# Kernel optimization log

Measured on AMD Instinct MI355X. Metric: run time of the kernel, lower is better.

Reference implementation:

```python
import jax, jax.numpy as jnp
import numpy as np
import math

FOV, NEAR, FAR = 60.0, 0.1, 100.0
W_RES, H_RES = 128, 128
N_GAUSS = 1024


def _normalize(v):
    return v / (jnp.linalg.norm(v) + 1e-8)


def _view_matrix(pos, look_at, up):
    # Same construction as Camera._compute_view_matrix
    f = _normalize(look_at - pos)
    r = _normalize(jnp.cross(f, up))
    u = _normalize(jnp.cross(r, f))
    return jnp.stack([
        jnp.concatenate([r, -jnp.dot(r, pos)[None]]),
        jnp.concatenate([u, -jnp.dot(u, pos)[None]]),
        jnp.concatenate([-f, jnp.dot(f, pos)[None]]),
        jnp.array([0.0, 0.0, 0.0, 1.0], dtype=pos.dtype),
    ])


def _proj_matrix():
    # Same construction as Camera._compute_projection_matrix
    aspect = W_RES / H_RES
    foc = 1.0 / math.tan(math.radians(FOV) / 2.0)
    P = np.zeros((4, 4), np.float32)
    P[0, 0] = foc / aspect
    P[1, 1] = foc
    P[2, 2] = (FAR + NEAR) / (NEAR - FAR)
    P[2, 3] = 2.0 * FAR * NEAR / (NEAR - FAR)
    P[3, 2] = -1.0
    return jnp.asarray(P)


def _quat_to_rot(q):
    # q: [N,4] (w,x,y,z) -> [N,3,3]
    q = q / (jnp.linalg.norm(q, axis=-1, keepdims=True) + 1e-8)
    w, x, y, z = q[:, 0], q[:, 1], q[:, 2], q[:, 3]
    return jnp.stack([
        jnp.stack([1 - 2 * (y * y + z * z), 2 * (x * y - w * z), 2 * (x * z + w * y)], -1),
        jnp.stack([2 * (x * y + w * z), 1 - 2 * (x * x + z * z), 2 * (y * z - w * x)], -1),
        jnp.stack([2 * (x * z - w * y), 2 * (y * z + w * x), 1 - 2 * (x * x + y * y)], -1),
    ], axis=1)


def _splat(means, log_scales, quats, opacity_logits, colors, cam_position, look_at, up):
    V = _view_matrix(cam_position, look_at, up)
    P = _proj_matrix()

    # 3D covariance: R S S^T R^T
    R = _quat_to_rot(quats)                       # [N,3,3]
    S = jnp.exp(log_scales)                       # [N,3]
    M = R * S[:, None, :]
    cov3d = jnp.einsum('nij,nkj->nik', M, M)      # [N,3,3]

    # Project means to view / clip / pixel space
    mh = jnp.concatenate([means, jnp.ones((means.shape[0], 1), means.dtype)], -1)
    pv = mh @ V.T                                 # [N,4] view space
    tx, ty, tz = pv[:, 0], pv[:, 1], pv[:, 2]     # tz < 0 in front of camera
    depth = -tz
    clip = pv @ P.T
    cw = jnp.where(jnp.abs(clip[:, 3]) < 1e-6, 1e-6, clip[:, 3])
    ndc = clip[:, :2] / cw[:, None]
    px = (ndc[:, 0] + 1.0) * 0.5 * W_RES          # pixel x center
    py = (ndc[:, 1] + 1.0) * 0.5 * H_RES          # pixel y center

    # EWA Jacobian -> 2D covariance
    foc = 1.0 / math.tan(math.radians(FOV) / 2.0)
    fx = foc / (W_RES / H_RES) * (W_RES / 2.0)
    fy = foc * (H_RES / 2.0)
    zsafe = jnp.where(jnp.abs(tz) < 1e-6, 1e-6, tz)
    zero = jnp.zeros_like(zsafe)
    J = jnp.stack([
        jnp.stack([fx / zsafe, zero, -fx * tx / (zsafe * zsafe)], -1),
        jnp.stack([zero, fy / zsafe, -fy * ty / (zsafe * zsafe)], -1),
    ], axis=1)                                    # [N,2,3]
    T = jnp.einsum('nij,jk->nik', J, V[:3, :3])   # [N,2,3]
    cov2d = jnp.einsum('nij,njk,nlk->nil', T, cov3d, T)  # [N,2,2]
    a = cov2d[:, 0, 0] + 0.3
    b = cov2d[:, 0, 1]
    c = cov2d[:, 1, 1] + 0.3
    det = jnp.maximum(a * c - b * b, 1e-6)
    ia, ib, ic = c / det, -b / det, a / det       # inverse 2x2

    # Per-pixel Gaussian weights: [N,H,W]
    u = jnp.arange(W_RES, dtype=means.dtype) + 0.5
    v = jnp.arange(H_RES, dtype=means.dtype) + 0.5
    dx = px[:, None, None] - u[None, None, :]
    dy = py[:, None, None] - v[None, :, None]
    power = -0.5 * (ia[:, None, None] * dx * dx
                    + 2.0 * ib[:, None, None] * dx * dy
                    + ic[:, None, None] * dy * dy)
    opac = jax.nn.sigmoid(opacity_logits)
    w = opac[:, None, None] * jnp.exp(jnp.minimum(power, 0.0))
    valid = (depth > NEAR) & (depth < FAR)
    w = jnp.where(valid[:, None, None], w, 0.0)
    w = jnp.clip(w, 0.0, 0.99)

    # Depth sort (front-to-back) then alpha composite via exclusive cumsum of log(1-a)
    order = jnp.argsort(depth)
    ws = w[order]                                 # [N,H,W]
    cs = jax.nn.sigmoid(colors)[order]            # [N,3]
    ds = depth[order]
    log_om = jnp.log1p(-ws)
    trans = jnp.exp(jnp.cumsum(log_om, axis=0) - log_om)  # exclusive transmittance
    contrib = trans * ws                          # [N,H,W]
    rgb = jnp.einsum('nhw,nc->chw', contrib, cs)  # [3,H,W]
    depth_img = jnp.sum(contrib * ds[:, None, None], axis=0, keepdims=True)
    alpha_img = jnp.sum(contrib, axis=0, keepdims=True)
    # background_color = [0,0,0] so no background term is added
    return rgb, depth_img, alpha_img


def setup_inputs() -> dict:
    key = jax.random.key(0)
    ks = jax.random.split(key, 6)
    means = jax.random.normal(ks[0], (N_GAUSS, 3), jnp.float32) * 1.5
    log_scales = jax.random.normal(ks[1], (N_GAUSS, 3), jnp.float32) * 0.3 - 2.5
    quats = jax.random.normal(ks[2], (N_GAUSS, 4), jnp.float32)
    opacity_logits = jax.random.normal(ks[3], (N_GAUSS,), jnp.float32)
    colors = jax.random.normal(ks[4], (N_GAUSS, 3), jnp.float32)
    cam_position = jnp.array([0.0, 0.0, 5.0], jnp.float32) + 0.05 * jax.random.normal(ks[5], (3,), jnp.float32)
    look_at = jnp.zeros((3,), jnp.float32)
    up = jnp.array([0.0, 1.0, 0.0], jnp.float32)
    return {"means": means, "log_scales": log_scales, "quats": quats,
            "opacity_logits": opacity_logits, "colors": colors,
            "cam_position": cam_position, "look_at": look_at, "up": up}


def reference(means, log_scales, quats, opacity_logits, colors, cam_position, look_at, up):
    return _splat(means, log_scales, quats, opacity_logits, colors, cam_position, look_at, up)
```

## Files before the change

### kernel.cpp

```cpp
#include <hip/hip_runtime.h>
#include <math.h>

#define NG 1024
#define W_RES 128
#define H_RES 128
#define NPIX (W_RES * H_RES)
#define NCHUNK 8
#define CH (NG / NCHUNK)
#define TILES_X 8
#define TILES_Y 8
#define NTILE (TILES_X * TILES_Y)

__device__ float  s_px[NG];
__device__ float  s_py[NG];
__device__ float  s_R2[NG];
__device__ float4 s_g0[NG];
__device__ float4 s_g1[NG];
__device__ float4 s_col[NG];
__device__ float  g_part[6 * NCHUNK * NPIX];

__global__ __launch_bounds__(128) void prep_kernel(
    const float* __restrict__ means, const float* __restrict__ log_scales,
    const float* __restrict__ quats, const float* __restrict__ opacity_logits,
    const float* __restrict__ colors, const float* __restrict__ cam,
    const float* __restrict__ look, const float* __restrict__ up) {
  __shared__ __align__(16) float sdepth[NG];
  const int tid = threadIdx.x;
  const int me = blockIdx.x * CH + tid;

  const float cpx = cam[0], cpy = cam[1], cpz = cam[2];
  float fx0 = look[0] - cpx, fy0 = look[1] - cpy, fz0 = look[2] - cpz;
  float inv = 1.f / (sqrtf(fx0 * fx0 + fy0 * fy0 + fz0 * fz0) + 1e-8f);
  const float fX = fx0 * inv, fY = fy0 * inv, fZ = fz0 * inv;
  const float ux0 = up[0], uy0 = up[1], uz0 = up[2];
  float rX0 = fY * uz0 - fZ * uy0, rY0 = fZ * ux0 - fX * uz0, rZ0 = fX * uy0 - fY * ux0;
  inv = 1.f / (sqrtf(rX0 * rX0 + rY0 * rY0 + rZ0 * rZ0) + 1e-8f);
  const float rX = rX0 * inv, rY = rY0 * inv, rZ = rZ0 * inv;
  float uX0 = rY * fZ - rZ * fY, uY0 = rZ * fX - rX * fZ, uZ0 = rX * fY - rY * fX;
  inv = 1.f / (sqrtf(uX0 * uX0 + uY0 * uY0 + uZ0 * uZ0) + 1e-8f);
  const float uX = uX0 * inv, uY = uY0 * inv, uZ = uZ0 * inv;
  const float V00 = rX, V01 = rY, V02 = rZ, V03 = -(rX * cpx + rY * cpy + rZ * cpz);
  const float V10 = uX, V11 = uY, V12 = uZ, V13 = -(uX * cpx + uY * cpy + uZ * cpz);
  const float V20 = -fX, V21 = -fY, V22 = -fZ, V23 = (fX * cpx + fY * cpy + fZ * cpz);

  const float foc = 1.7320508075688772f;
  const float fpx = foc * 64.f;
  const float fpy = foc * 64.f;

#pragma unroll
  for (int i = 0; i < NG / CH; ++i) {
    const int g = i * CH + tid;
    const float mx = means[3 * g + 0], my = means[3 * g + 1], mz = means[3 * g + 2];
    sdepth[g] = -(V20 * mx + V21 * my + V22 * mz + V23);
  }
  __syncthreads();

  const float dme = sdepth[me];
  int rank = 0;
  const float4* dep4 = (const float4*)sdepth;
#pragma unroll 4
  for (int k = 0; k < NG / 4; ++k) {
    const float4 d4 = dep4[k];
    const int j = 4 * k;
    rank += (d4.x < dme || (d4.x == dme && (j + 0) < me)) ? 1 : 0;
    rank += (d4.y < dme || (d4.y == dme && (j + 1) < me)) ? 1 : 0;
    rank += (d4.z < dme || (d4.z == dme && (j + 2) < me)) ? 1 : 0;
    rank += (d4.w < dme || (d4.w == dme && (j + 3) < me)) ? 1 : 0;
  }

  float qw = quats[4 * me + 0], qx = quats[4 * me + 1], qy = quats[4 * me + 2], qz = quats[4 * me + 3];
  float qinv = 1.f / (sqrtf(qw * qw + qx * qx + qy * qy + qz * qz) + 1e-8f);
  qw *= qinv; qx *= qinv; qy *= qinv; qz *= qinv;
  const float R00 = 1.f - 2.f * (qy * qy + qz * qz), R01 = 2.f * (qx * qy - qw * qz), R02 = 2.f * (qx * qz + qw * qy);
  const float R10 = 2.f * (qx * qy + qw * qz), R11 = 1.f - 2.f * (qx * qx + qz * qz), R12 = 2.f * (qy * qz - qw * qx);
  const float R20 = 2.f * (qx * qz - qw * qy), R21 = 2.f * (qy * qz + qw * qx), R22 = 1.f - 2.f * (qx * qx + qy * qy);
  const float s0 = __expf(log_scales[3 * me + 0]);
  const float s1 = __expf(log_scales[3 * me + 1]);
  const float s2 = __expf(log_scales[3 * me + 2]);
  const float M00 = R00 * s0, M01 = R01 * s1, M02 = R02 * s2;
  const float M10 = R10 * s0, M11 = R11 * s1, M12 = R12 * s2;
  const float M20 = R20 * s0, M21 = R21 * s1, M22 = R22 * s2;
  const float c00 = M00 * M00 + M01 * M01 + M02 * M02;
  const float c01 = M00 * M10 + M01 * M11 + M02 * M12;
  const float c02 = M00 * M20 + M01 * M21 + M02 * M22;
  const float c11 = M10 * M10 + M11 * M11 + M12 * M12;
  const float c12 = M10 * M20 + M11 * M21 + M12 * M22;
  const float c22 = M20 * M20 + M21 * M21 + M22 * M22;
  const float mx = means[3 * me + 0], my = means[3 * me + 1], mz = means[3 * me + 2];
  const float tx = V00 * mx + V01 * my + V02 * mz + V03;
  const float ty = V10 * mx + V11 * my + V12 * mz + V13;
  const float tz = V20 * mx + V21 * my + V22 * mz + V23;
  const float depth = -tz;
  const float cw = (fabsf(depth) < 1e-6f) ? 1e-6f : depth;
  const float pxs = (foc * tx / cw + 1.f) * 0.5f * (float)W_RES;
  const float pys = (foc * ty / cw + 1.f) * 0.5f * (float)H_RES;
  const float zs = (fabsf(tz) < 1e-6f) ? 1e-6f : tz;
  const float J00 = fpx / zs, J02 = -fpx * tx / (zs * zs);
  const float J11 = fpy / zs, J12 = -fpy * ty / (zs * zs);
  const float T00 = J00 * V00 + J02 * V20;
  const float T01 = J00 * V01 + J02 * V21;
  const float T02 = J00 * V02 + J02 * V22;
  const float T10 = J11 * V10 + J12 * V20;
  const float T11 = J11 * V11 + J12 * V21;
  const float T12 = J11 * V12 + J12 * V22;
  const float t00 = T00 * c00 + T01 * c01 + T02 * c02;
  const float t01 = T00 * c01 + T01 * c11 + T02 * c12;
  const float t02 = T00 * c02 + T01 * c12 + T02 * c22;
  const float t10 = T10 * c00 + T11 * c01 + T12 * c02;
  const float t11 = T10 * c01 + T11 * c11 + T12 * c12;
  const float t12 = T10 * c02 + T11 * c12 + T12 * c22;
  const float a  = t00 * T00 + t01 * T01 + t02 * T02 + 0.3f;
  const float bb = t00 * T10 + t01 * T11 + t02 * T12;
  const float c  = t10 * T10 + t11 * T11 + t12 * T12 + 0.3f;
  const float det = fmaxf(a * c - bb * bb, 1e-6f);
  const float ia = c / det, ib = -bb / det, ic = a / det;
  const float op = 1.f / (1.f + __expf(-opacity_logits[me]));
  const bool valid = (depth > 0.1f) && (depth < 100.f);
  const float lam = 0.5f * (a + c) + sqrtf(0.25f * (a - c) * (a - c) + bb * bb);
  float R2v = 2.f * lam * logf(op * 1e7f);
  if (!valid) R2v = -1.f;
  const float logop = logf(op);
  const float cr = 1.f / (1.f + __expf(-colors[3 * me + 0]));
  const float cg = 1.f / (1.f + __expf(-colors[3 * me + 1]));
  const float cb = 1.f / (1.f + __expf(-colors[3 * me + 2]));

  s_px[rank] = pxs;
  s_py[rank] = pys;
  s_R2[rank] = R2v;
  s_g0[rank] = make_float4(pxs, pys, -0.5f * ia, -ib);
  s_g1[rank] = make_float4(-0.5f * ic, logop, depth, 0.f);
  s_col[rank] = make_float4(cr, cg, cb, 0.f);
}

__global__ __launch_bounds__(256) void render_kernel() {
  __shared__ int slist[CH];
  __shared__ int scnt[2];
  __shared__ int stotal;
  const int tid = threadIdx.x;
  const int tile = blockIdx.x;
  const int chunk = blockIdx.y;
  const int ox = (tile & (TILES_X - 1)) * 16;
  const int oy = (tile >> 3) * 16;
  const float x0 = ox + 0.5f, x1 = ox + 15.5f;
  const float y0 = oy + 0.5f, y1 = oy + 15.5f;

  bool surv = false;
  if (tid < CH) {
    const int g = chunk * CH + tid;
    const float gx = s_px[g], gy = s_py[g], r2 = s_R2[g];
    const float nx = fminf(fmaxf(gx, x0), x1);
    const float ny = fminf(fmaxf(gy, y0), y1);
    const float ddx = nx - gx, ddy = ny - gy;
    surv = (ddx * ddx + ddy * ddy) <= r2;
  }
  const unsigned long long m = __ballot(surv);
  const int wid = tid >> 6, lane = tid & 63;
  if (tid < CH && lane == 0) scnt[wid] = __popcll(m);
  __syncthreads();
  if (surv) {
    const int base = (wid == 1) ? scnt[0] : 0;
    const int pos = base + __popcll(m & ((1ull << lane) - 1ull));
    slist[pos] = chunk * CH + tid;
  }
  if (tid == 0) stotal = scnt[0] + scnt[1];
  __syncthreads();
  const int ns = stotal;

  const int lx = tid & 15, ly = tid >> 4;
  const float u = (float)(ox + lx) + 0.5f;
  const float v = (float)(oy + ly) + 0.5f;
  float T = 1.f, ar = 0.f, ag = 0.f, ab = 0.f, ad = 0.f, aa = 0.f;
  for (int s = 0; s < ns; ++s) {
    const int g = slist[s];
    const float4 g0 = s_g0[g];
    const float4 g1 = s_g1[g];
    const float4 cc = s_col[g];
    const float dx = g0.x - u, dy = g0.y - v;
    float pw = dx * (g0.z * dx + g0.w * dy) + g1.x * dy * dy;
    pw = fminf(pw, 0.f) + g1.y;
    const float w = fminf(__expf(pw), 0.99f);
    const float ctr = T * w;
    ar += ctr * cc.x; ag += ctr * cc.y; ab += ctr * cc.z;
    ad += ctr * g1.z; aa += ctr;
    T *= (1.f - w);
  }
  const int p = (oy + ly) * W_RES + (ox + lx);
  const int idx = chunk * NPIX + p;
  g_part[0 * NCHUNK * NPIX + idx] = ar;
  g_part[1 * NCHUNK * NPIX + idx] = ag;
  g_part[2 * NCHUNK * NPIX + idx] = ab;
  g_part[3 * NCHUNK * NPIX + idx] = ad;
  g_part[4 * NCHUNK * NPIX + idx] = aa;
  g_part[5 * NCHUNK * NPIX + idx] = T;
}

__global__ __launch_bounds__(256) void combine_kernel(float* __restrict__ out) {
  const int p = blockIdx.x * 256 + threadIdx.x;
  float T = 1.f, r = 0.f, g = 0.f, b = 0.f, d = 0.f, a = 0.f;
#pragma unroll
  for (int ch = 0; ch < NCHUNK; ++ch) {
    const int idx = ch * NPIX + p;
    const float pr = g_part[0 * NCHUNK * NPIX + idx];
    const float pg = g_part[1 * NCHUNK * NPIX + idx];
    const float pb = g_part[2 * NCHUNK * NPIX + idx];
    const float pd = g_part[3 * NCHUNK * NPIX + idx];
    const float pa = g_part[4 * NCHUNK * NPIX + idx];
    const float pT = g_part[5 * NCHUNK * NPIX + idx];
    r += T * pr; g += T * pg; b += T * pb; d += T * pd; a += T * pa;
    T *= pT;
  }
  out[0 * NPIX + p] = r;
  out[1 * NPIX + p] = g;
  out[2 * NPIX + p] = b;
  out[3 * NPIX + p] = d;
  out[4 * NPIX + p] = a;
}

extern "C" void kernel_launch(void* const* d_in, const int* in_sizes, int n_in,
                              void* d_out, int out_size, void* d_ws, size_t ws_size,
                              hipStream_t stream) {
  const float* means = (const float*)d_in[0];
  const float* log_scales = (const float*)d_in[1];
  const float* quats = (const float*)d_in[2];
  const float* opacity_logits = (const float*)d_in[3];
  const float* colors = (const float*)d_in[4];
  const float* cam = (const float*)d_in[5];
  const float* look = (const float*)d_in[6];
  const float* up = (const float*)d_in[7];
  float* out = (float*)d_out;

  prep_kernel<<<NCHUNK, CH, 0, stream>>>(means, log_scales, quats, opacity_logits,
                                         colors, cam, look, up);
  render_kernel<<<dim3(NTILE, NCHUNK), 256, 0, stream>>>();
  combine_kernel<<<NPIX / 256, 256, 0, stream>>>(out);
}
```

Measured before the change: 106.9 us.

## Render each tile over all gaussians in one block, drop combine kernel

The render kernel no longer splits the gaussians into 8 chunks across blocks. Each tile block now culls all 1024 depth-sorted gaussians and compacts the survivors' parameters into shared memory. It then composites them and writes the final output directly, which removes the partial-result buffer and the combine kernel launch. The cost is only 64 blocks on a large GPU and a longer serial compositing loop per pixel, in exchange for one fewer launch, less global traffic and no indirect gather.

```diff
diff --git a/kernel.cpp b/kernel.cpp
--- a/kernel.cpp
+++ b/kernel.cpp
@@ -5,19 +5,15 @@
 #define W_RES 128
 #define H_RES 128
 #define NPIX (W_RES * H_RES)
-#define NCHUNK 8
-#define CH (NG / NCHUNK)
+#define NBLK 8
+#define BT (NG / NBLK)
 #define TILES_X 8
-#define TILES_Y 8
-#define NTILE (TILES_X * TILES_Y)
-
-__device__ float  s_px[NG];
-__device__ float  s_py[NG];
+#define NTILE 64
+
 __device__ float  s_R2[NG];
 __device__ float4 s_g0[NG];
 __device__ float4 s_g1[NG];
 __device__ float4 s_col[NG];
-__device__ float  g_part[6 * NCHUNK * NPIX];
 
 __global__ __launch_bounds__(128) void prep_kernel(
     const float* __restrict__ means, const float* __restrict__ log_scales,
@@ -26,7 +22,7 @@
     const float* __restrict__ look, const float* __restrict__ up) {
   __shared__ __align__(16) float sdepth[NG];
   const int tid = threadIdx.x;
-  const int me = blockIdx.x * CH + tid;
+  const int me = blockIdx.x * BT + tid;
 
   const float cpx = cam[0], cpy = cam[1], cpz = cam[2];
   float fx0 = look[0] - cpx, fy0 = look[1] - cpy, fz0 = look[2] - cpz;
@@ -48,8 +44,8 @@
   const float fpy = foc * 64.f;
 
 #pragma unroll
-  for (int i = 0; i < NG / CH; ++i) {
-    const int g = i * CH + tid;
+  for (int i = 0; i < NG / BT; ++i) {
+    const int g = i * BT + tid;
     const float mx = means[3 * g + 0], my = means[3 * g + 1], mz = means[3 * g + 2];
     sdepth[g] = -(V20 * mx + V21 * my + V22 * mz + V23);
   }
@@ -124,57 +120,58 @@
   const float cg = 1.f / (1.f + __expf(-colors[3 * me + 1]));
   const float cb = 1.f / (1.f + __expf(-colors[3 * me + 2]));
 
-  s_px[rank] = pxs;
-  s_py[rank] = pys;
-  s_R2[rank] = R2v;
-  s_g0[rank] = make_float4(pxs, pys, -0.5f * ia, -ib);
-  s_g1[rank] = make_float4(-0.5f * ic, logop, depth, 0.f);
+  s_R2[rank]  = R2v;
+  s_g0[rank]  = make_float4(pxs, pys, -0.5f * ia, -ib);
+  s_g1[rank]  = make_float4(-0.5f * ic, logop, depth, 0.f);
   s_col[rank] = make_float4(cr, cg, cb, 0.f);
 }
 
-__global__ __launch_bounds__(256) void render_kernel() {
-  __shared__ int slist[CH];
-  __shared__ int scnt[2];
-  __shared__ int stotal;
+__global__ __launch_bounds__(256) void render_kernel(float* __restrict__ out) {
+  __shared__ float4 tg0[NG];
+  __shared__ float4 tg1[NG];
+  __shared__ float4 tcol[NG];
+  __shared__ int scnt[4];
   const int tid = threadIdx.x;
   const int tile = blockIdx.x;
-  const int chunk = blockIdx.y;
+  const int wid = tid >> 6, lane = tid & 63;
   const int ox = (tile & (TILES_X - 1)) * 16;
   const int oy = (tile >> 3) * 16;
   const float x0 = ox + 0.5f, x1 = ox + 15.5f;
   const float y0 = oy + 0.5f, y1 = oy + 15.5f;
 
-  bool surv = false;
-  if (tid < CH) {
-    const int g = chunk * CH + tid;
-    const float gx = s_px[g], gy = s_py[g], r2 = s_R2[g];
-    const float nx = fminf(fmaxf(gx, x0), x1);
-    const float ny = fminf(fmaxf(gy, y0), y1);
-    const float ddx = nx - gx, ddy = ny - gy;
-    surv = (ddx * ddx + ddy * ddy) <= r2;
-  }
-  const unsigned long long m = __ballot(surv);
-  const int wid = tid >> 6, lane = tid & 63;
-  if (tid < CH && lane == 0) scnt[wid] = __popcll(m);
-  __syncthreads();
-  if (surv) {
-    const int base = (wid == 1) ? scnt[0] : 0;
-    const int pos = base + __popcll(m & ((1ull << lane) - 1ull));
-    slist[pos] = chunk * CH + tid;
-  }
-  if (tid == 0) stotal = scnt[0] + scnt[1];
-  __syncthreads();
-  const int ns = stotal;
+  int total = 0;
+#pragma unroll
+  for (int r = 0; r < 4; ++r) {
+    const int g = r * 256 + tid;
+    const float4 g0 = s_g0[g];
+    const float r2 = s_R2[g];
+    const float nx = fminf(fmaxf(g0.x, x0), x1);
+    const float ny = fminf(fmaxf(g0.y, y0), y1);
+    const float ddx = nx - g0.x, ddy = ny - g0.y;
+    const bool surv = (ddx * ddx + ddy * ddy) <= r2;
+    const unsigned long long m = __ballot(surv);
+    if (lane == 0) scnt[wid] = __popcll(m);
+    __syncthreads();
+    int base = total;
+    for (int w = 0; w < wid; ++w) base += scnt[w];
+    total += scnt[0] + scnt[1] + scnt[2] + scnt[3];
+    if (surv) {
+      const int pos = base + __popcll(m & ((1ull << lane) - 1ull));
+      tg0[pos] = g0;
+      tg1[pos] = s_g1[g];
+      tcol[pos] = s_col[g];
+    }
+    __syncthreads();
+  }
 
   const int lx = tid & 15, ly = tid >> 4;
   const float u = (float)(ox + lx) + 0.5f;
   const float v = (float)(oy + ly) + 0.5f;
   float T = 1.f, ar = 0.f, ag = 0.f, ab = 0.f, ad = 0.f, aa = 0.f;
-  for (int s = 0; s < ns; ++s) {
-    const int g = slist[s];
-    const float4 g0 = s_g0[g];
-    const float4 g1 = s_g1[g];
-    const float4 cc = s_col[g];
+  for (int s = 0; s < total; ++s) {
+    const float4 g0 = tg0[s];
+    const float4 g1 = tg1[s];
+    const float4 cc = tcol[s];
     const float dx = g0.x - u, dy = g0.y - v;
     float pw = dx * (g0.z * dx + g0.w * dy) + g1.x * dy * dy;
     pw = fminf(pw, 0.f) + g1.y;
@@ -185,35 +182,11 @@
     T *= (1.f - w);
   }
   const int p = (oy + ly) * W_RES + (ox + lx);
-  const int idx = chunk * NPIX + p;
-  g_part[0 * NCHUNK * NPIX + idx] = ar;
-  g_part[1 * NCHUNK * NPIX + idx] = ag;
-  g_part[2 * NCHUNK * NPIX + idx] = ab;
-  g_part[3 * NCHUNK * NPIX + idx] = ad;
-  g_part[4 * NCHUNK * NPIX + idx] = aa;
-  g_part[5 * NCHUNK * NPIX + idx] = T;
-}
-
-__global__ __launch_bounds__(256) void combine_kernel(float* __restrict__ out) {
-  const int p = blockIdx.x * 256 + threadIdx.x;
-  float T = 1.f, r = 0.f, g = 0.f, b = 0.f, d = 0.f, a = 0.f;
-#pragma unroll
-  for (int ch = 0; ch < NCHUNK; ++ch) {
-    const int idx = ch * NPIX + p;
-    const float pr = g_part[0 * NCHUNK * NPIX + idx];
-    const float pg = g_part[1 * NCHUNK * NPIX + idx];
-    const float pb = g_part[2 * NCHUNK * NPIX + idx];
-    const float pd = g_part[3 * NCHUNK * NPIX + idx];
-    const float pa = g_part[4 * NCHUNK * NPIX + idx];
-    const float pT = g_part[5 * NCHUNK * NPIX + idx];
-    r += T * pr; g += T * pg; b += T * pb; d += T * pd; a += T * pa;
-    T *= pT;
-  }
-  out[0 * NPIX + p] = r;
-  out[1 * NPIX + p] = g;
-  out[2 * NPIX + p] = b;
-  out[3 * NPIX + p] = d;
-  out[4 * NPIX + p] = a;
+  out[0 * NPIX + p] = ar;
+  out[1 * NPIX + p] = ag;
+  out[2 * NPIX + p] = ab;
+  out[3 * NPIX + p] = ad;
+  out[4 * NPIX + p] = aa;
 }
 
 extern "C" void kernel_launch(void* const* d_in, const int* in_sizes, int n_in,
@@ -229,8 +202,7 @@
   const float* up = (const float*)d_in[7];
   float* out = (float*)d_out;
 
-  prep_kernel<<<NCHUNK, CH, 0, stream>>>(means, log_scales, quats, opacity_logits,
-                                         colors, cam, look, up);
-  render_kernel<<<dim3(NTILE, NCHUNK), 256, 0, stream>>>();
-  combine_kernel<<<NPIX / 256, 256, 0, stream>>>(out);
+  prep_kernel<<<NBLK, BT, 0, stream>>>(means, log_scales, quats, opacity_logits,
+                                       colors, cam, look, up);
+  render_kernel<<<NTILE, 256, 0, stream>>>(out);
 }
```

Result: slower. 111.0 us (+3.9%).
